# Kernel tuning notes

Hardware: AMD Instinct MI355X
Metric: run time of the kernel (lower is better)

Reference implementation:

```python
import jax, jax.numpy as jnp
import numpy as np


def setup_inputs() -> dict:
    key = jax.random.key(0)
    k1, k2, k3 = jax.random.split(key, 3)
    N, C_in, H, W = 32, 128, 112, 112
    C_out, Hf, Wf = 256, 3, 3
    k = float(np.sqrt(1.0 / (C_in * Hf * Wf)))
    img = jax.random.normal(k1, (N, C_in, H, W), dtype=jnp.float32)
    weight = jax.random.uniform(k2, (C_out, C_in, Hf, Wf), minval=-k, maxval=k, dtype=jnp.float32)
    bias = jax.random.uniform(k3, (C_out,), minval=-k, maxval=k, dtype=jnp.float32)
    return {"img": img, "weight": weight, "bias": bias}


def reference(img, weight, bias):
    # Equivalent to the torch module's im2col + GEMM conv2d with stride 1, pad 1,
    # zeros padding mode. Expressed as a direct convolution (same math).
    out = jax.lax.conv_general_dilated(
        img, weight,
        window_strides=(1, 1),
        padding=((1, 1), (1, 1)),
        dimension_numbers=("NCHW", "OIHW", "NCHW"),
    )
    return out + bias[None, :, None, None]
```

## Files before the change

### kernel.cpp

```cpp
#include <hip/hip_runtime.h>

typedef unsigned int u32;
typedef unsigned short u16;
typedef float f32x4 __attribute__((ext_vector_type(4)));
typedef __bf16 bf16x8 __attribute__((ext_vector_type(8)));

#define N_IMG 32
#define C_IN 128
#define HW_DIM 112
#define C_OUT 256
#define PADD 114
#define PIX_PER_IMG (HW_DIM * HW_DIM)
#define NPIX (N_IMG * PIX_PER_IMG)
#define KTOT 1152
#define IBUF_BYTES ((size_t)N_IMG * PADD * PADD * C_IN * 2)

__device__ __forceinline__ u16 f2bf(float f) {
  u32 u = __builtin_bit_cast(u32, f);
  u32 r = u + 0x7fffu + ((u >> 16) & 1u);
  return (u16)(r >> 16);
}

__device__ __forceinline__ void async16(const void* g, void* l) {
  __builtin_amdgcn_global_load_lds(
      (const __attribute__((address_space(1))) u32*)g,
      (__attribute__((address_space(3))) u32*)l, 16, 0, 0);
}

__global__ __launch_bounds__(256) void zero_border(u16* __restrict__ buf) {
  int g = blockIdx.x * 256 + threadIdx.x;
  int n = g / (452 * 128);
  int r = g % (452 * 128);
  int pix = r >> 7;
  int ci = r & 127;
  int h, w;
  if (pix < 114)      { h = 0;         w = pix; }
  else if (pix < 228) { h = 113;       w = pix - 114; }
  else if (pix < 340) { h = pix - 227; w = 0; }
  else                { h = pix - 339; w = 113; }
  buf[((size_t)(n * PADD + h) * PADD + w) * C_IN + ci] = 0;
}

__global__ __launch_bounds__(256) void convert_input(const float* __restrict__ in,
                                                     u16* __restrict__ buf) {
  __shared__ u32 lds[64 * 65];
  int tid = threadIdx.x;
  int b = blockIdx.x;
  int n = b / 196;
  int hwb = (b % 196) * 64;
  int lw = tid & 63;
  int wv = tid >> 6;
  const float* src = in + (size_t)n * C_IN * PIX_PER_IMG + hwb + lw;
#pragma unroll
  for (int cb = 0; cb < 4; ++cb)
#pragma unroll
    for (int j = 0; j < 4; ++j) {
      int c = cb * 16 + wv * 4 + j;
      float f0 = src[(size_t)(2 * c) * PIX_PER_IMG];
      float f1 = src[(size_t)(2 * c + 1) * PIX_PER_IMG];
      lds[lw * 65 + c] = (u32)f2bf(f0) | ((u32)f2bf(f1) << 16);
    }
  __syncthreads();
#pragma unroll
  for (int k = 0; k < 4; ++k) {
    int g = k * 256 + tid;
    int row = g >> 4, ch = g & 15;
    u32 d0 = lds[row * 65 + ch * 4 + 0];
    u32 d1 = lds[row * 65 + ch * 4 + 1];
    u32 d2 = lds[row * 65 + ch * 4 + 2];
    u32 d3 = lds[row * 65 + ch * 4 + 3];
    int hw = hwb + row;
    int h = hw / HW_DIM, w = hw % HW_DIM;
    u32* dst = (u32*)(buf + ((size_t)(n * PADD + h + 1) * PADD + (w + 1)) * C_IN) + ch * 4;
    uint4 v; v.x = d0; v.y = d1; v.z = d2; v.w = d3;
    *(uint4*)dst = v;
  }
}

__global__ __launch_bounds__(256) void convert_weight(const float* __restrict__ w,
                                                      u16* __restrict__ wt) {
  int g = blockIdx.x * 256 + threadIdx.x;
  int co = g / KTOT;
  int r = g % KTOT;
  int f = r >> 7;
  int ci = r & 127;
  wt[g] = f2bf(w[(size_t)(co * C_IN + ci) * 9 + f]);
}

__global__ __launch_bounds__(256) void conv_mfma(const u16* __restrict__ ibuf,
                                                 const u16* __restrict__ wbuf,
                                                 const float* __restrict__ bias,
                                                 float* __restrict__ out) {
  __shared__ __attribute__((aligned(16))) char smem[16384 * 2 + 1024];
  char* ldsA = smem;
  char* ldsB = smem + 16384;
  float* ldsBias = (float*)(smem + 32768);

  int tid = threadIdx.x;
  int lane = tid & 63;
  int wv = tid >> 6;
  int bi0 = blockIdx.x;
  int bi = (bi0 & 7) * 784 + (bi0 >> 3);
  int co_tile = bi & 1;
  int pix_tile = bi >> 1;
  int pb = pix_tile * 128;
  int co_base = co_tile * 128;

  ldsBias[tid] = bias[tid];

  const char* gA[4];
  const char* gB[4];
#pragma unroll
  for (int j = 0; j < 4; ++j) {
    int r = j * 32 + (tid >> 3);
    int cg = (tid & 7) ^ (r & 7);
    gA[j] = (const char*)wbuf + (size_t)(co_base + r) * (KTOT * 2) + cg * 16;
    int pid = pb + r;
    int n = pid / PIX_PER_IMG;
    int hw = pid % PIX_PER_IMG;
    int h = hw / HW_DIM, w = hw % HW_DIM;
    gB[j] = (const char*)ibuf + ((size_t)(n * PADD + h) * PADD + w) * (C_IN * 2) + cg * 16;
  }

  f32x4 acc[4][4] = {};
  int wm = wv & 1;
  int wn = wv >> 1;
  int q = lane >> 4;
  int lr = lane & 15;

  for (int s = 0; s < 18; ++s) {
    __syncthreads();
    int offA = s * 128;
    int f = s >> 1;
    int kh = (f * 11) >> 5;
    int kw = f - kh * 3;
    int offB = (kh * PADD + kw) * (C_IN * 2) + (s & 1) * 128;
#pragma unroll
    for (int j = 0; j < 4; ++j) {
      async16(gA[j] + offA, ldsA + (j * 256 + wv * 64) * 16);
      async16(gB[j] + offB, ldsB + (j * 256 + wv * 64) * 16);
    }
    __syncthreads();
#pragma unroll
    for (int kb = 0; kb < 2; ++kb) {
      bf16x8 af[4], bf[4];
#pragma unroll
      for (int mt = 0; mt < 4; ++mt) {
        int row = wm * 64 + mt * 16 + lr;
        int ch = (kb * 4 + q) ^ (row & 7);
        af[mt] = *(const bf16x8*)(ldsA + row * 128 + ch * 16);
      }
#pragma unroll
      for (int nt = 0; nt < 4; ++nt) {
        int row = wn * 64 + nt * 16 + lr;
        int ch = (kb * 4 + q) ^ (row & 7);
        bf[nt] = *(const bf16x8*)(ldsB + row * 128 + ch * 16);
      }
#pragma unroll
      for (int mt = 0; mt < 4; ++mt)
#pragma unroll
        for (int nt = 0; nt < 4; ++nt)
          acc[mt][nt] = __builtin_amdgcn_mfma_f32_16x16x32_bf16(af[mt], bf[nt], acc[mt][nt], 0, 0, 0);
    }
  }

  int n_img = pb / PIX_PER_IMG;
  int hw_base = pb % PIX_PER_IMG;
  float* outp = out + (size_t)n_img * C_OUT * PIX_PER_IMG + hw_base;
#pragma unroll
  for (int mt = 0; mt < 4; ++mt) {
    int co0 = co_base + wm * 64 + mt * 16 + q * 4;
    float4 bv = *(const float4*)&ldsBias[co0];
    const float* bvp = (const float*)&bv;
#pragma unroll
    for (int nt = 0; nt < 4; ++nt) {
      int pix = wn * 64 + nt * 16 + lr;
#pragma unroll
      for (int r = 0; r < 4; ++r)
        outp[(size_t)(co0 + r) * PIX_PER_IMG + pix] = acc[mt][nt][r] + bvp[r];
    }
  }
}

extern "C" void kernel_launch(void* const* d_in, const int* in_sizes, int n_in,
                              void* d_out, int out_size, void* d_ws, size_t ws_size,
                              hipStream_t stream) {
  (void)in_sizes; (void)n_in; (void)out_size; (void)ws_size;
  const float* img = (const float*)d_in[0];
  const float* wgt = (const float*)d_in[1];
  const float* bias = (const float*)d_in[2];
  float* out = (float*)d_out;
  u16* ibuf = (u16*)d_ws;
  u16* wbuf = (u16*)((char*)d_ws + IBUF_BYTES);

  zero_border<<<7232, 256, 0, stream>>>(ibuf);
  convert_input<<<6272, 256, 0, stream>>>(img, ibuf);
  convert_weight<<<1152, 256, 0, stream>>>(wgt, wbuf);
  conv_mfma<<<6272, 256, 0, stream>>>(ibuf, wbuf, bias, out);
}
```

Before: 808.4 us.

## Double-buffer LDS tiles with async prefetch two stages ahead in conv MFMA

Replaces the single-buffered load/compute loop with two LDS buffers, so each K-stage is issued two iterations ahead and waited on with explicit vmcnt counts. The goal is to hide global-to-LDS latency behind the MFMA work. It also raises wave priority during the MFMA block and reads bias straight from global memory instead of staging it in LDS. LDS use grows to 64 KB per block, which may cut occupancy, and correctness now depends on the hand-set vmcnt values.

```diff
diff --git a/kernel.cpp b/kernel.cpp
--- a/kernel.cpp
+++ b/kernel.cpp
@@ -91,10 +91,7 @@
                                                  const u16* __restrict__ wbuf,
                                                  const float* __restrict__ bias,
                                                  float* __restrict__ out) {
-  __shared__ __attribute__((aligned(16))) char smem[16384 * 2 + 1024];
-  char* ldsA = smem;
-  char* ldsB = smem + 16384;
-  float* ldsBias = (float*)(smem + 32768);
+  __shared__ __attribute__((aligned(16))) char smem[65536];
 
   int tid = threadIdx.x;
   int lane = tid & 63;
@@ -106,8 +103,6 @@
   int pb = pix_tile * 128;
   int co_base = co_tile * 128;
 
-  ldsBias[tid] = bias[tid];
-
   const char* gA[4];
   const char* gB[4];
 #pragma unroll
@@ -122,25 +117,42 @@
     gB[j] = (const char*)ibuf + ((size_t)(n * PADD + h) * PADD + w) * (C_IN * 2) + cg * 16;
   }
 
+#define STAGE(t, buf)                                                          \
+  do {                                                                         \
+    int offA_ = (t) * 128;                                                     \
+    int f_ = (t) >> 1;                                                         \
+    int kh_ = (f_ * 11) >> 5;                                                  \
+    int kw_ = f_ - kh_ * 3;                                                    \
+    int offB_ = (kh_ * PADD + kw_) * (C_IN * 2) + ((t) & 1) * 128;             \
+    char* dA_ = smem + (buf) * 32768;                                          \
+    char* dB_ = dA_ + 16384;                                                   \
+    _Pragma("unroll")                                                          \
+    for (int j_ = 0; j_ < 4; ++j_) {                                           \
+      async16(gA[j_] + offA_, dA_ + (j_ * 256 + wv * 64) * 16);                \
+      async16(gB[j_] + offB_, dB_ + (j_ * 256 + wv * 64) * 16);                \
+    }                                                                          \
+  } while (0)
+
   f32x4 acc[4][4] = {};
   int wm = wv & 1;
   int wn = wv >> 1;
   int q = lane >> 4;
   int lr = lane & 15;
 
-  for (int s = 0; s < 18; ++s) {
-    __syncthreads();
-    int offA = s * 128;
-    int f = s >> 1;
-    int kh = (f * 11) >> 5;
-    int kw = f - kh * 3;
-    int offB = (kh * PADD + kw) * (C_IN * 2) + (s & 1) * 128;
-#pragma unroll
-    for (int j = 0; j < 4; ++j) {
-      async16(gA[j] + offA, ldsA + (j * 256 + wv * 64) * 16);
-      async16(gB[j] + offB, ldsB + (j * 256 + wv * 64) * 16);
-    }
-    __syncthreads();
+  STAGE(0, 0);
+  STAGE(1, 1);
+
+  for (int t = 0; t < 18; ++t) {
+    int cur = t & 1;
+    if (t == 17) { asm volatile("s_waitcnt vmcnt(0)" ::: "memory"); }
+    else         { asm volatile("s_waitcnt vmcnt(8)" ::: "memory"); }
+    __builtin_amdgcn_sched_barrier(0);
+    __builtin_amdgcn_s_barrier();
+    __builtin_amdgcn_sched_barrier(0);
+
+    const char* lA = smem + cur * 32768;
+    const char* lB = lA + 16384;
+    __builtin_amdgcn_s_setprio(1);
 #pragma unroll
     for (int kb = 0; kb < 2; ++kb) {
       bf16x8 af[4], bf[4];
@@ -148,13 +160,13 @@
       for (int mt = 0; mt < 4; ++mt) {
         int row = wm * 64 + mt * 16 + lr;
         int ch = (kb * 4 + q) ^ (row & 7);
-        af[mt] = *(const bf16x8*)(ldsA + row * 128 + ch * 16);
+        af[mt] = *(const bf16x8*)(lA + row * 128 + ch * 16);
       }
 #pragma unroll
       for (int nt = 0; nt < 4; ++nt) {
         int row = wn * 64 + nt * 16 + lr;
         int ch = (kb * 4 + q) ^ (row & 7);
-        bf[nt] = *(const bf16x8*)(ldsB + row * 128 + ch * 16);
+        bf[nt] = *(const bf16x8*)(lB + row * 128 + ch * 16);
       }
 #pragma unroll
       for (int mt = 0; mt < 4; ++mt)
@@ -162,7 +174,14 @@
         for (int nt = 0; nt < 4; ++nt)
           acc[mt][nt] = __builtin_amdgcn_mfma_f32_16x16x32_bf16(af[mt], bf[nt], acc[mt][nt], 0, 0, 0);
     }
-  }
+    __builtin_amdgcn_s_setprio(0);
+    __builtin_amdgcn_sched_barrier(0);
+    __builtin_amdgcn_s_barrier();
+    __builtin_amdgcn_sched_barrier(0);
+    if (t + 2 < 18) STAGE(t + 2, cur);
+    __builtin_amdgcn_sched_barrier(0);
+  }
+#undef STAGE
 
   int n_img = pb / PIX_PER_IMG;
   int hw_base = pb % PIX_PER_IMG;
@@ -170,7 +189,7 @@
 #pragma unroll
   for (int mt = 0; mt < 4; ++mt) {
     int co0 = co_base + wm * 64 + mt * 16 + q * 4;
-    float4 bv = *(const float4*)&ldsBias[co0];
+    float4 bv = *(const float4*)&bias[co0];
     const float* bvp = (const float*)&bv;
 #pragma unroll
     for (int nt = 0; nt < 4; ++nt) {
```

Result: faster. 753.5 us (-6.8%).
